# Kernel tuning notes

Hardware: AMD Instinct MI355X
Metric: run time of the kernel (lower is better)

Reference implementation:

```python
import jax, jax.numpy as jnp
import numpy as np

NUM_FORMULAS = 1024
INPUT_DIM = 256
BATCH = 2048


def setup_inputs() -> dict:
    key = jax.random.key(0)
    k_x, k_mu, k_sigma = jax.random.split(key, 3)
    inputs = jax.random.normal(k_x, (BATCH, INPUT_DIM), dtype=jnp.float32)
    # keras random_normal initializer default stddev = 0.05
    mu = 0.05 * jax.random.normal(k_mu, (NUM_FORMULAS, INPUT_DIM), dtype=jnp.float32)
    sigma = 0.05 * jax.random.normal(k_sigma, (1, NUM_FORMULAS, INPUT_DIM), dtype=jnp.float32)
    temperature = jnp.float32(2.0)
    return {"inputs": inputs, "mu": mu, "sigma": sigma, "temperature": temperature}


def reference(inputs, mu, sigma, temperature):
    # diff: (batch, num_formulas, dim)
    diff = inputs[:, None, :] - mu[None, :, :]
    # weighted L2 norm over feature dim -> (batch, num_formulas)
    dist = jnp.sqrt(jnp.sum(jnp.square(diff * sigma), axis=-1))
    loc = jnp.exp(-dist)
    # sigmoid-gated temperature, softmax over formulas (last axis)
    return jax.nn.softmax(jax.nn.sigmoid(temperature) * loc, axis=-1)
```

## Files before the change

### kernel.cpp

```cpp
#include <hip/hip_runtime.h>
#include <math.h>

#define NF 1024
#define DIM 256
#define BATCH 2048
#define K 512
#define BMF 16
#define NCC 4
#define CF (NF / NCC)
#define KS 32
#define NSTEP (K / KS)

#define WS_C_OFF  (NF * K * 2)
#define WS_RP_OFF (WS_C_OFF + NF * 4)

typedef __attribute__((ext_vector_type(8))) short short8;
typedef __attribute__((ext_vector_type(4))) float f32x4;

__device__ __forceinline__ unsigned short f2bf(float f) {
    unsigned u = __float_as_uint(f);
    u += 0x7fffu + ((u >> 16) & 1u);
    return (unsigned short)(u >> 16);
}

__global__ __launch_bounds__(256) void k_prep(const float* __restrict__ mu,
                                              const float* __restrict__ sigma,
                                              uint4* __restrict__ Bb4,
                                              float* __restrict__ c) {
    const int t = threadIdx.x;
    const int f = blockIdx.x * 4 + (t >> 6);
    const int sq = t & 63;
    const float4 mv = *(const float4*)&mu[f * DIM + sq * 4];
    const float4 sv = *(const float4*)&sigma[f * DIM + sq * 4];

    uint4 pk; float cp = 0.f;
    {
        const float s2x = sv.x * sv.x;
        pk.x = (unsigned)f2bf(s2x) | ((unsigned)f2bf(-2.0f * s2x * mv.x) << 16);
        cp += s2x * mv.x * mv.x;
        const float s2y = sv.y * sv.y;
        pk.y = (unsigned)f2bf(s2y) | ((unsigned)f2bf(-2.0f * s2y * mv.y) << 16);
        cp += s2y * mv.y * mv.y;
        const float s2z = sv.z * sv.z;
        pk.z = (unsigned)f2bf(s2z) | ((unsigned)f2bf(-2.0f * s2z * mv.z) << 16);
        cp += s2z * mv.z * mv.z;
        const float s2w = sv.w * sv.w;
        pk.w = (unsigned)f2bf(s2w) | ((unsigned)f2bf(-2.0f * s2w * mv.w) << 16);
        cp += s2w * mv.w * mv.w;
    }
    Bb4[(f >> 8) * 16384 + (sq >> 2) * 1024 + (sq & 3) * 256 + (f & 255)] = pk;

    #pragma unroll
    for (int off = 32; off > 0; off >>= 1) cp += __shfl_down(cp, off, 64);
    if ((t & 63) == 0) c[f] = cp;
}

__global__ __launch_bounds__(256, 2) void k_main(const float* __restrict__ x,
                                                 const ushort* __restrict__ Bb,
                                                 const float* __restrict__ c,
                                                 const float* __restrict__ temp,
                                                 float* __restrict__ out,
                                                 float* __restrict__ rowPartial) {
    const int t = threadIdx.x;
    const int w = t >> 6;
    const int lane = t & 63;
    const int m16 = lane & 15;
    const int q = lane >> 4;
    const int r0 = blockIdx.x * BMF;
    const int cc = blockIdx.y;

    __shared__ __align__(16) ushort ldsA[BMF * K];
    __shared__ float wsum[4][BMF];

    #pragma unroll
    for (int h = 0; h < 4; ++h) {
        const int u = h * 256 + t;
        const int row = u >> 6, kc = u & 63;
        const float4 v = *(const float4*)&x[(r0 + row) * DIM + kc * 4];
        uint4 pk;
        pk.x = (unsigned)f2bf(v.x * v.x) | ((unsigned)f2bf(v.x) << 16);
        pk.y = (unsigned)f2bf(v.y * v.y) | ((unsigned)f2bf(v.y) << 16);
        pk.z = (unsigned)f2bf(v.z * v.z) | ((unsigned)f2bf(v.z) << 16);
        pk.w = (unsigned)f2bf(v.w * v.w) | ((unsigned)f2bf(v.w) << 16);
        *(uint4*)&ldsA[(row * 64 + (kc ^ (row & 7))) * 8] = pk;
    }

    f32x4 acc[4];
    #pragma unroll
    for (int ct = 0; ct < 4; ++ct) acc[ct] = (f32x4){0.f, 0.f, 0.f, 0.f};

    const ushort* bp = Bb + cc * (CF * K) + q * (CF * 8) + (w * 64 + m16) * 8;

    short8 bA[4], bB[4];
    #pragma unroll
    for (int ct = 0; ct < 4; ++ct)
        bA[ct] = *(const short8*)(bp + ct * 128);

    __syncthreads();

    #pragma unroll 1
    for (int s = 0; s < NSTEP; s += 2) {
        #pragma unroll
        for (int ct = 0; ct < 4; ++ct)
            bB[ct] = *(const short8*)(bp + (s + 1) * 8192 + ct * 128);
        {
            const int kcq = s * 4 + q;
            const short8 av = *(const short8*)&ldsA[(m16 * 64 + (kcq ^ (m16 & 7))) * 8];
            #pragma unroll
            for (int ct = 0; ct < 4; ++ct)
                acc[ct] = __builtin_amdgcn_mfma_f32_16x16x32_bf16(av, bA[ct], acc[ct], 0, 0, 0);
        }
        if (s + 2 < NSTEP) {
            #pragma unroll
            for (int ct = 0; ct < 4; ++ct)
                bA[ct] = *(const short8*)(bp + (s + 2) * 8192 + ct * 128);
        }
        {
            const int kcq = (s + 1) * 4 + q;
            const short8 av = *(const short8*)&ldsA[(m16 * 64 + (kcq ^ (m16 & 7))) * 8];
            #pragma unroll
            for (int ct = 0; ct < 4; ++ct)
                acc[ct] = __builtin_amdgcn_mfma_f32_16x16x32_bf16(av, bB[ct], acc[ct], 0, 0, 0);
        }
    }

    const float g = 1.0f / (1.0f + __expf(-temp[0]));
    float s4[4] = {0.f, 0.f, 0.f, 0.f};
    #pragma unroll
    for (int ct = 0; ct < 4; ++ct) {
        const int fcol = cc * CF + w * 64 + ct * 16 + m16;
        const float cn = c[fcol];
        #pragma unroll
        for (int i = 0; i < 4; ++i) {
            const float dist2 = acc[ct][i] + cn;
            const float dist = sqrtf(fmaxf(dist2, 0.0f));
            const float p = __expf(g * __expf(-dist));
            out[(r0 + q * 4 + i) * NF + fcol] = p;
            s4[i] += p;
        }
    }
    #pragma unroll
    for (int i = 0; i < 4; ++i) {
        #pragma unroll
        for (int mask = 1; mask < 16; mask <<= 1)
            s4[i] += __shfl_xor(s4[i], mask, 64);
    }
    if (m16 == 0) {
        #pragma unroll
        for (int i = 0; i < 4; ++i) wsum[w][q * 4 + i] = s4[i];
    }
    __syncthreads();
    if (t < BMF)
        rowPartial[cc * BATCH + r0 + t] =
            (wsum[0][t] + wsum[1][t]) + (wsum[2][t] + wsum[3][t]);
}

__global__ __launch_bounds__(256) void k_norm(float* __restrict__ out,
                                              const float* __restrict__ rowPartial) {
    const int row = blockIdx.x;
    const float ssum = (rowPartial[row] + rowPartial[BATCH + row]) +
                       (rowPartial[2 * BATCH + row] + rowPartial[3 * BATCH + row]);
    const float inv = 1.0f / ssum;
    float4* o4 = (float4*)(out + row * NF);
    float4 v = o4[threadIdx.x];
    v.x *= inv; v.y *= inv; v.z *= inv; v.w *= inv;
    o4[threadIdx.x] = v;
}

extern "C" void kernel_launch(void* const* d_in, const int* in_sizes, int n_in,
                              void* d_out, int out_size, void* d_ws, size_t ws_size,
                              hipStream_t stream) {
    const float* x     = (const float*)d_in[0];
    const float* mu    = (const float*)d_in[1];
    const float* sigma = (const float*)d_in[2];
    const float* temp  = (const float*)d_in[3];
    float* out = (float*)d_out;

    char* ws = (char*)d_ws;
    ushort* Bb         = (ushort*)ws;
    float*  c          = (float*)(ws + WS_C_OFF);
    float*  rowPartial = (float*)(ws + WS_RP_OFF);

    k_prep<<<NF / 4, 256, 0, stream>>>(mu, sigma, (uint4*)Bb, c);

    dim3 g2(BATCH / BMF, NCC);
    k_main<<<g2, 256, 0, stream>>>(x, Bb, c, temp, out, rowPartial);

    k_norm<<<BATCH, 256, 0, stream>>>(out, rowPartial);
}
```

Measured before the change: 77.70 us.

## Fuse softmax normalization into main kernel via last-block atomic counter

Removes the separate normalization kernel. Each row-group counts finished column-chunk blocks with an atomic counter that k_prep resets. The last block to finish reads the four partial row sums and rescales its 16 output rows in place. This saves a kernel launch and lets the rescale pass overlap with other blocks, while the output is more likely still in cache. In exchange it adds a threadfence, an atomic and a serial 16-row loop in the tail blocks.

Result: slower. 135.1 us (+73.8%).

```diff
diff --git a/kernel.cpp b/kernel.cpp
--- a/kernel.cpp
+++ b/kernel.cpp
@@ -10,9 +10,11 @@
 #define CF (NF / NCC)
 #define KS 32
 #define NSTEP (K / KS)
-
-#define WS_C_OFF  (NF * K * 2)
-#define WS_RP_OFF (WS_C_OFF + NF * 4)
+#define NRG (BATCH / BMF)
+
+#define WS_C_OFF   (NF * K * 2)
+#define WS_RP_OFF  (WS_C_OFF + NF * 4)
+#define WS_CNT_OFF (WS_RP_OFF + NCC * BATCH * 4)
 
 typedef __attribute__((ext_vector_type(8))) short short8;
 typedef __attribute__((ext_vector_type(4))) float f32x4;
@@ -26,8 +28,11 @@
 __global__ __launch_bounds__(256) void k_prep(const float* __restrict__ mu,
                                               const float* __restrict__ sigma,
                                               uint4* __restrict__ Bb4,
-                                              float* __restrict__ c) {
+                                              float* __restrict__ c,
+                                              int* __restrict__ cnt) {
     const int t = threadIdx.x;
+    if (blockIdx.x < NRG && t == 0) cnt[blockIdx.x] = 0;
+
     const int f = blockIdx.x * 4 + (t >> 6);
     const int sq = t & 63;
     const float4 mv = *(const float4*)&mu[f * DIM + sq * 4];
@@ -60,17 +65,21 @@
                                                  const float* __restrict__ c,
                                                  const float* __restrict__ temp,
                                                  float* __restrict__ out,
-                                                 float* __restrict__ rowPartial) {
+                                                 float* __restrict__ rowPartial,
+                                                 int* __restrict__ cnt) {
     const int t = threadIdx.x;
     const int w = t >> 6;
     const int lane = t & 63;
     const int m16 = lane & 15;
     const int q = lane >> 4;
-    const int r0 = blockIdx.x * BMF;
+    const int rg = blockIdx.x;
+    const int r0 = rg * BMF;
     const int cc = blockIdx.y;
 
     __shared__ __align__(16) ushort ldsA[BMF * K];
     __shared__ float wsum[4][BMF];
+    __shared__ float rowInvS[BMF];
+    __shared__ int sLast;
 
     #pragma unroll
     for (int h = 0; h < 4; ++h) {
@@ -153,18 +162,29 @@
     if (t < BMF)
         rowPartial[cc * BATCH + r0 + t] =
             (wsum[0][t] + wsum[1][t]) + (wsum[2][t] + wsum[3][t]);
-}
-
-__global__ __launch_bounds__(256) void k_norm(float* __restrict__ out,
-                                              const float* __restrict__ rowPartial) {
-    const int row = blockIdx.x;
-    const float ssum = (rowPartial[row] + rowPartial[BATCH + row]) +
-                       (rowPartial[2 * BATCH + row] + rowPartial[3 * BATCH + row]);
-    const float inv = 1.0f / ssum;
-    float4* o4 = (float4*)(out + row * NF);
-    float4 v = o4[threadIdx.x];
-    v.x *= inv; v.y *= inv; v.z *= inv; v.w *= inv;
-    o4[threadIdx.x] = v;
+
+    __threadfence();
+    __syncthreads();
+    if (t == 0) sLast = (atomicAdd(&cnt[rg], 1) == NCC - 1);
+    __syncthreads();
+    if (!sLast) return;
+
+    __threadfence();
+    if (t < BMF) {
+        const int row = r0 + t;
+        const float ssum = (rowPartial[row] + rowPartial[BATCH + row]) +
+                           (rowPartial[2 * BATCH + row] + rowPartial[3 * BATCH + row]);
+        rowInvS[t] = 1.0f / ssum;
+    }
+    __syncthreads();
+    #pragma unroll 1
+    for (int row = 0; row < BMF; ++row) {
+        const float inv = rowInvS[row];
+        float4* o4 = (float4*)(out + (r0 + row) * NF);
+        float4 v = o4[t];
+        v.x *= inv; v.y *= inv; v.z *= inv; v.w *= inv;
+        o4[t] = v;
+    }
 }
 
 extern "C" void kernel_launch(void* const* d_in, const int* in_sizes, int n_in,
@@ -180,11 +200,10 @@
     ushort* Bb         = (ushort*)ws;
     float*  c          = (float*)(ws + WS_C_OFF);
     float*  rowPartial = (float*)(ws + WS_RP_OFF);
-
-    k_prep<<<NF / 4, 256, 0, stream>>>(mu, sigma, (uint4*)Bb, c);
+    int*    cnt        = (int*)(ws + WS_CNT_OFF);
+
+    k_prep<<<NF / 4, 256, 0, stream>>>(mu, sigma, (uint4*)Bb, c, cnt);
 
     dim3 g2(BATCH / BMF, NCC);
-    k_main<<<g2, 256, 0, stream>>>(x, Bb, c, temp, out, rowPartial);
-
-    k_norm<<<BATCH, 256, 0, stream>>>(out, rowPartial);
-}
+    k_main<<<g2, 256, 0, stream>>>(x, Bb, c, temp, out, rowPartial, cnt);
+}
```

## Fuse softmax normalization into main kernel with full-row 1024-thread blocks

Applied to the files above, without the earlier changes.

Each block now covers all 1024 formulas for its 16 rows with 16 waves instead of splitting formulas across 4 column blocks. This lets the block compute the row sums itself, keep the exp values in registers, and write normalized outputs directly. The separate normalization kernel and its 8 MB read-modify-write of the output go away, along with the rowPartial buffer. The grid shrinks to 128 blocks of 1024 threads, which may underfill the GPU's CUs and adds a block-wide barrier before the stores.

Measured after the change: 75.41 us (median of 2 runs). 1.03x faster.

```diff
diff --git a/kernel.cpp b/kernel.cpp
--- a/kernel.cpp
+++ b/kernel.cpp
@@ -6,13 +6,10 @@
 #define BATCH 2048
 #define K 512
 #define BMF 16
-#define NCC 4
-#define CF (NF / NCC)
 #define KS 32
 #define NSTEP (K / KS)
 
-#define WS_C_OFF  (NF * K * 2)
-#define WS_RP_OFF (WS_C_OFF + NF * 4)
+#define WS_C_OFF (NF * K * 2)
 
 typedef __attribute__((ext_vector_type(8))) short short8;
 typedef __attribute__((ext_vector_type(4))) float f32x4;
@@ -48,34 +45,31 @@
         pk.w = (unsigned)f2bf(s2w) | ((unsigned)f2bf(-2.0f * s2w * mv.w) << 16);
         cp += s2w * mv.w * mv.w;
     }
-    Bb4[(f >> 8) * 16384 + (sq >> 2) * 1024 + (sq & 3) * 256 + (f & 255)] = pk;
+    Bb4[(sq >> 2) * 4096 + (sq & 3) * 1024 + f] = pk;
 
     #pragma unroll
     for (int off = 32; off > 0; off >>= 1) cp += __shfl_down(cp, off, 64);
     if ((t & 63) == 0) c[f] = cp;
 }
 
-__global__ __launch_bounds__(256, 2) void k_main(const float* __restrict__ x,
-                                                 const ushort* __restrict__ Bb,
-                                                 const float* __restrict__ c,
-                                                 const float* __restrict__ temp,
-                                                 float* __restrict__ out,
-                                                 float* __restrict__ rowPartial) {
+__global__ __launch_bounds__(1024, 1) void k_fused(const float* __restrict__ x,
+                                                   const ushort* __restrict__ Bb,
+                                                   const float* __restrict__ c,
+                                                   const float* __restrict__ temp,
+                                                   float* __restrict__ out) {
     const int t = threadIdx.x;
     const int w = t >> 6;
     const int lane = t & 63;
     const int m16 = lane & 15;
     const int q = lane >> 4;
     const int r0 = blockIdx.x * BMF;
-    const int cc = blockIdx.y;
 
     __shared__ __align__(16) ushort ldsA[BMF * K];
-    __shared__ float wsum[4][BMF];
+    __shared__ float wsum[16][BMF];
+    __shared__ float rowInv[BMF];
 
-    #pragma unroll
-    for (int h = 0; h < 4; ++h) {
-        const int u = h * 256 + t;
-        const int row = u >> 6, kc = u & 63;
+    {
+        const int row = t >> 6, kc = t & 63;
         const float4 v = *(const float4*)&x[(r0 + row) * DIM + kc * 4];
         uint4 pk;
         pk.x = (unsigned)f2bf(v.x * v.x) | ((unsigned)f2bf(v.x) << 16);
@@ -89,7 +83,7 @@
     #pragma unroll
     for (int ct = 0; ct < 4; ++ct) acc[ct] = (f32x4){0.f, 0.f, 0.f, 0.f};
 
-    const ushort* bp = Bb + cc * (CF * K) + q * (CF * 8) + (w * 64 + m16) * 8;
+    const ushort* bp = Bb + q * (NF * 8) + (w * 64 + m16) * 8;
 
     short8 bA[4], bB[4];
     #pragma unroll
@@ -102,7 +96,7 @@
     for (int s = 0; s < NSTEP; s += 2) {
         #pragma unroll
         for (int ct = 0; ct < 4; ++ct)
-            bB[ct] = *(const short8*)(bp + (s + 1) * 8192 + ct * 128);
+            bB[ct] = *(const short8*)(bp + (s + 1) * (NF * KS) + ct * 128);
         {
             const int kcq = s * 4 + q;
             const short8 av = *(const short8*)&ldsA[(m16 * 64 + (kcq ^ (m16 & 7))) * 8];
@@ -113,7 +107,7 @@
         if (s + 2 < NSTEP) {
             #pragma unroll
             for (int ct = 0; ct < 4; ++ct)
-                bA[ct] = *(const short8*)(bp + (s + 2) * 8192 + ct * 128);
+                bA[ct] = *(const short8*)(bp + (s + 2) * (NF * KS) + ct * 128);
         }
         {
             const int kcq = (s + 1) * 4 + q;
@@ -128,14 +122,13 @@
     float s4[4] = {0.f, 0.f, 0.f, 0.f};
     #pragma unroll
     for (int ct = 0; ct < 4; ++ct) {
-        const int fcol = cc * CF + w * 64 + ct * 16 + m16;
-        const float cn = c[fcol];
+        const float cn = c[w * 64 + ct * 16 + m16];
         #pragma unroll
         for (int i = 0; i < 4; ++i) {
             const float dist2 = acc[ct][i] + cn;
             const float dist = sqrtf(fmaxf(dist2, 0.0f));
             const float p = __expf(g * __expf(-dist));
-            out[(r0 + q * 4 + i) * NF + fcol] = p;
+            acc[ct][i] = p;
             s4[i] += p;
         }
     }
@@ -150,21 +143,24 @@
         for (int i = 0; i < 4; ++i) wsum[w][q * 4 + i] = s4[i];
     }
     __syncthreads();
-    if (t < BMF)
-        rowPartial[cc * BATCH + r0 + t] =
-            (wsum[0][t] + wsum[1][t]) + (wsum[2][t] + wsum[3][t]);
-}
+    if (t < BMF) {
+        float ssum = 0.f;
+        #pragma unroll
+        for (int ww = 0; ww < 16; ++ww) ssum += wsum[ww][t];
+        rowInv[t] = 1.0f / ssum;
+    }
+    __syncthreads();
 
-__global__ __launch_bounds__(256) void k_norm(float* __restrict__ out,
-                                              const float* __restrict__ rowPartial) {
-    const int row = blockIdx.x;
-    const float ssum = (rowPartial[row] + rowPartial[BATCH + row]) +
-                       (rowPartial[2 * BATCH + row] + rowPartial[3 * BATCH + row]);
-    const float inv = 1.0f / ssum;
-    float4* o4 = (float4*)(out + row * NF);
-    float4 v = o4[threadIdx.x];
-    v.x *= inv; v.y *= inv; v.z *= inv; v.w *= inv;
-    o4[threadIdx.x] = v;
+    float inv[4];
+    #pragma unroll
+    for (int i = 0; i < 4; ++i) inv[i] = rowInv[q * 4 + i];
+    #pragma unroll
+    for (int ct = 0; ct < 4; ++ct) {
+        const int fcol = w * 64 + ct * 16 + m16;
+        #pragma unroll
+        for (int i = 0; i < 4; ++i)
+            out[(r0 + q * 4 + i) * NF + fcol] = acc[ct][i] * inv[i];
+    }
 }
 
 extern "C" void kernel_launch(void* const* d_in, const int* in_sizes, int n_in,
@@ -177,14 +173,9 @@
     float* out = (float*)d_out;
 
     char* ws = (char*)d_ws;
-    ushort* Bb         = (ushort*)ws;
-    float*  c          = (float*)(ws + WS_C_OFF);
-    float*  rowPartial = (float*)(ws + WS_RP_OFF);
+    ushort* Bb = (ushort*)ws;
+    float*  c  = (float*)(ws + WS_C_OFF);
 
     k_prep<<<NF / 4, 256, 0, stream>>>(mu, sigma, (uint4*)Bb, c);
-
-    dim3 g2(BATCH / BMF, NCC);
-    k_main<<<g2, 256, 0, stream>>>(x, Bb, c, temp, out, rowPartial);
-
-    k_norm<<<BATCH, 256, 0, stream>>>(out, rowPartial);
+    k_fused<<<BATCH / BMF, 1024, 0, stream>>>(x, Bb, c, temp, out);
 }
```
